# Performance work log

Measured on AMD Instinct MI355X. Metric: run time of the kernel, lower is better.

The kernel has to match this reference:

```python
import jax, jax.numpy as jnp
import numpy as np

N_NODES = 50000
N_EDGES = 1250000
IN_CH = 64
HID = 64
N_CLASSES = 10
N_GRAPHS = 128


def _xavier(key, shape):
    fan_out, fan_in = shape
    limit = np.sqrt(6.0 / (fan_in + fan_out))
    return jax.random.uniform(key, shape, jnp.float32, -limit, limit)


def setup_inputs() -> dict:
    key = jax.random.key(0)
    ks = jax.random.split(key, 12)
    x = jax.random.normal(ks[0], (N_NODES, IN_CH), jnp.float32)
    edge_index = jax.random.randint(ks[1], (2, N_EDGES), 0, N_NODES, jnp.int64)
    batch = jnp.sort(jax.random.randint(ks[2], (N_NODES,), 0, N_GRAPHS, jnp.int64))
    return {
        "x": x,
        "edge_index": edge_index,
        "batch": batch,
        # GraphConv i: lin_rel (weight+bias) applied to aggregated neighbors,
        # lin_root (no bias) applied to self features. Weights are [out, in].
        "W1_rel": _xavier(ks[3], (HID, IN_CH)), "b1": jnp.zeros((HID,), jnp.float32),
        "W1_root": _xavier(ks[4], (HID, IN_CH)),
        "W2_rel": _xavier(ks[5], (HID, HID)), "b2": jnp.zeros((HID,), jnp.float32),
        "W2_root": _xavier(ks[6], (HID, HID)),
        "W3_rel": _xavier(ks[7], (HID, HID)), "b3": jnp.zeros((HID,), jnp.float32),
        "W3_root": _xavier(ks[8], (HID, HID)),
        "W_lin": _xavier(ks[9], (N_CLASSES, HID)), "b_lin": jnp.zeros((N_CLASSES,), jnp.float32),
    }


def _graph_conv(x, src, dst, W_rel, b, W_root):
    # sum-aggregate neighbor features: gather at src, scatter-add at dst
    agg = jax.ops.segment_sum(x[src], dst, num_segments=N_NODES)  # [N, F]
    return agg @ W_rel.T + b + x @ W_root.T


def reference(x, edge_index, batch, W1_rel, b1, W1_root, W2_rel, b2, W2_root,
              W3_rel, b3, W3_root, W_lin, b_lin):
    src, dst = edge_index[0], edge_index[1]
    h = jax.nn.relu(_graph_conv(x, src, dst, W1_rel, b1, W1_root))
    h = jax.nn.relu(_graph_conv(h, src, dst, W2_rel, b2, W2_root))
    h = _graph_conv(h, src, dst, W3_rel, b3, W3_root)
    # global mean pool over graphs
    sums = jax.ops.segment_sum(h, batch, num_segments=N_GRAPHS)        # [G, HID]
    counts = jax.ops.segment_sum(jnp.ones((h.shape[0],), h.dtype), batch,
                                 num_segments=N_GRAPHS)
    pooled = sums / jnp.maximum(counts, 1.0)[:, None]
    out = pooled @ W_lin.T + b_lin  # dropout inactive in eval mode
    return (pooled, out)
```

## Files before the change

### kernel.cpp

```cpp
#include <hip/hip_runtime.h>

#define N_NODES   50000
#define HID       64
#define N_GRAPHS  128
#define N_CLASSES 10
#define NP        196
#define EPA       8192
#define PCAP      8192

typedef __attribute__((ext_vector_type(8))) short short8;
typedef __attribute__((ext_vector_type(4))) float f32x4;

__device__ __forceinline__ unsigned bf16rne(float f) {
    unsigned u = __float_as_uint(f);
    return (u + 0x7fffu + ((u >> 16) & 1u)) >> 16;
}
__device__ __forceinline__ unsigned pack_bf16x2(float lo, float hi) {
    return bf16rne(lo) | (bf16rne(hi) << 16);
}



__global__ void cvt_kernel(const float* __restrict__ x, unsigned short* __restrict__ xb,
                           int* __restrict__ gcursor) {
    if (blockIdx.x == 0 && threadIdx.x < NP) gcursor[threadIdx.x] = 0;
    int i = blockIdx.x * blockDim.x + threadIdx.x;
    if (i < N_NODES * 16) {
        float4 v = ((const float4*)x)[i];
        uint2 o;
        o.x = pack_bf16x2(v.x, v.y);
        o.y = pack_bf16x2(v.z, v.w);
        ((uint2*)xb)[i] = o;
    }
}


__global__ __launch_bounds__(256) void bucket_kernel(
    const int* __restrict__ src, const int* __restrict__ dst,
    int* __restrict__ gcursor, unsigned* __restrict__ packed, int E) {
    __shared__ int hist[NP], scp[NP], base[NP], cnt2[NP];
    __shared__ int sc[256];
    __shared__ unsigned stag[EPA];
    const int t = threadIdx.x;
    const int e0 = blockIdx.x * EPA;
    const int e1 = min(e0 + EPA, E);
    for (int i = t; i < NP; i += 256) { hist[i] = 0; cnt2[i] = 0; }
    __syncthreads();
    for (int e = e0 + t; e < e1; e += 256)
        atomicAdd(&hist[dst[e] >> 8], 1);
    __syncthreads();
    sc[t] = (t < NP) ? hist[t] : 0;
    __syncthreads();
    for (int off = 1; off < 256; off <<= 1) {
        int add = (t >= off) ? sc[t - off] : 0;
        __syncthreads();
        sc[t] += add;
        __syncthreads();
    }
    if (t < NP) {
        scp[t] = sc[t] - hist[t];
        if (hist[t] > 0) base[t] = atomicAdd(&gcursor[t], hist[t]);
    }
    __syncthreads();
    for (int e = e0 + t; e < e1; e += 256) {
        int d = dst[e], s = src[e];
        int p = d >> 8;
        int idx = scp[p] + atomicAdd(&cnt2[p], 1);
        stag[idx] = (unsigned)s | ((unsigned)(d & 255) << 16) | ((unsigned)p << 24);
    }
    __syncthreads();
    const int n = e1 - e0;
    for (int i = t; i < n; i += 256) {
        unsigned v = stag[i];
        int p = v >> 24;
        packed[(size_t)p * PCAP + base[p] + (i - scp[p])] = v & 0x00FFFFFFu;
    }
}

__global__ __launch_bounds__(256) void build_kernel(
    const unsigned* __restrict__ packed, const int* __restrict__ gcursor,
    int* __restrict__ offsets, unsigned short* __restrict__ csr,
    int* __restrict__ sums_zero) {
    __shared__ int hist[256], lofs[256], cnt[256], sc[256], gv[256];
    __shared__ unsigned short lcsr[PCAP];
    const int p = blockIdx.x, t = threadIdx.x;

    if (p == 0) {
        for (int i = t; i < N_GRAPHS * 64 + N_GRAPHS; i += 256) sums_zero[i] = 0;
    }

    int v = (t < NP) ? gcursor[t] : 0;
    sc[t] = v; gv[t] = v;
    __syncthreads();
    for (int off = 1; off < 256; off <<= 1) {
        int add = (t >= off) ? sc[t - off] : 0;
        __syncthreads();
        sc[t] += add;
        __syncthreads();
    }
    const int pb = sc[p] - gv[p];
    const int ne = gv[p];
    if (p == NP - 1 && t == 0) offsets[N_NODES] = sc[NP - 1];
    __syncthreads();

    const unsigned* mypk = packed + (size_t)p * PCAP;
    hist[t] = 0; cnt[t] = 0;
    __syncthreads();
    for (int i = t; i < ne; i += 256)
        atomicAdd(&hist[(mypk[i] >> 16) & 255], 1);
    __syncthreads();
    sc[t] = hist[t];
    __syncthreads();
    for (int off = 1; off < 256; off <<= 1) {
        int add = (t >= off) ? sc[t - off] : 0;
        __syncthreads();
        sc[t] += add;
        __syncthreads();
    }
    lofs[t] = sc[t] - hist[t];
    int node = p * 256 + t;
    if (node < N_NODES) offsets[node] = pb + lofs[t];
    __syncthreads();
    for (int i = t; i < ne; i += 256) {
        unsigned vv = mypk[i];
        int dl = (vv >> 16) & 255;
        int slot = lofs[dl] + atomicAdd(&cnt[dl], 1);
        lcsr[slot] = (unsigned short)(vv & 0xFFFFu);
    }
    __syncthreads();
    for (int i = t; i < ne; i += 256) csr[pb + i] = lcsr[i];
}


__global__ __launch_bounds__(256) void gather_kernel(
    const unsigned short* __restrict__ hin,
    const int* __restrict__ offsets, const unsigned short* __restrict__ csr_src,
    unsigned short* __restrict__ agg) {
    const int w = threadIdx.x >> 6, lane = threadIdx.x & 63;
    const int half = lane >> 5, hl = lane & 31;
    const int n = blockIdx.x * 4 + w;
    const int beg = offsets[n], end = offsets[n + 1];

    float accx = 0.f, accy = 0.f;
    for (int base = beg; base < end; base += 64) {
        int cnt = min(64, end - base);
        int sidx = (base + lane < end) ? (int)csr_src[base + lane] : 0;
        for (int kb = 0; kb < cnt; kb += 32) {
            unsigned u[16];
#pragma unroll
            for (int p = 0; p < 16; ++p) {
                int e = kb + 2 * p + half;
                int r = __shfl(sidx, e);
                u[p] = (e < cnt) ? *((const unsigned*)(hin + (size_t)r * 64) + hl) : 0u;
            }
#pragma unroll
            for (int p = 0; p < 16; ++p) {
                accx += __uint_as_float(u[p] << 16);
                accy += __uint_as_float(u[p] & 0xffff0000u);
            }
        }
    }
    float ox = accx + __shfl(accx, lane ^ 32);
    float oy = accy + __shfl(accy, lane ^ 32);
    if (half == 0)
        *((unsigned*)(agg + (size_t)n * 64) + hl) = pack_bf16x2(ox, oy);
}


template <int RELU>
__global__ __launch_bounds__(256) void linear_kernel(
    const unsigned short* __restrict__ agg,
    const unsigned short* __restrict__ hin,
    const float* __restrict__ Wrel, const float* __restrict__ bias,
    const float* __restrict__ Wroot, unsigned short* __restrict__ hout) {
    __shared__ unsigned short outT[4][16][72];

    const int tid = threadIdx.x;
    const int w = tid >> 6, lane = tid & 63;
    const int q = lane >> 4, c = lane & 15;
    const int g0 = (blockIdx.x * 4 + w) * 16;
    if (g0 >= N_NODES) return;

    short8 brel[4][2], broot[4][2];
    float biasv[4];
#pragma unroll
    for (int t = 0; t < 4; ++t) {
        int o = t * 16 + c;
        biasv[t] = bias[o];
#pragma unroll
        for (int s = 0; s < 2; ++s) {
            const float4* pr = (const float4*)(Wrel  + o * 64 + s * 32 + q * 8);
            const float4* po = (const float4*)(Wroot + o * 64 + s * 32 + q * 8);
            float4 r0 = pr[0], r1 = pr[1], z0 = po[0], z1 = po[1];
            short8 rr, zz;
            rr[0] = (short)bf16rne(r0.x); rr[1] = (short)bf16rne(r0.y);
            rr[2] = (short)bf16rne(r0.z); rr[3] = (short)bf16rne(r0.w);
            rr[4] = (short)bf16rne(r1.x); rr[5] = (short)bf16rne(r1.y);
            rr[6] = (short)bf16rne(r1.z); rr[7] = (short)bf16rne(r1.w);
            zz[0] = (short)bf16rne(z0.x); zz[1] = (short)bf16rne(z0.y);
            zz[2] = (short)bf16rne(z0.z); zz[3] = (short)bf16rne(z0.w);
            zz[4] = (short)bf16rne(z1.x); zz[5] = (short)bf16rne(z1.y);
            zz[6] = (short)bf16rne(z1.z); zz[7] = (short)bf16rne(z1.w);
            brel[t][s] = rr; broot[t][s] = zz;
        }
    }

    const int na = min(g0 + c, N_NODES - 1);
    short8 a_agg[2], a_x[2];
#pragma unroll
    for (int s = 0; s < 2; ++s) {
        a_agg[s] = *(const short8*)(agg + (size_t)na * 64 + s * 32 + q * 8);
        a_x[s]   = *(const short8*)(hin + (size_t)na * 64 + s * 32 + q * 8);
    }

    f32x4 acc4[4];
#pragma unroll
    for (int t = 0; t < 4; ++t) {
        f32x4 a0 = {biasv[t], biasv[t], biasv[t], biasv[t]};
        a0 = __builtin_amdgcn_mfma_f32_16x16x32_bf16(a_agg[0], brel[t][0], a0, 0, 0, 0);
        a0 = __builtin_amdgcn_mfma_f32_16x16x32_bf16(a_agg[1], brel[t][1], a0, 0, 0, 0);
        a0 = __builtin_amdgcn_mfma_f32_16x16x32_bf16(a_x[0],  broot[t][0], a0, 0, 0, 0);
        a0 = __builtin_amdgcn_mfma_f32_16x16x32_bf16(a_x[1],  broot[t][1], a0, 0, 0, 0);
        acc4[t] = a0;
    }

#pragma unroll
    for (int t = 0; t < 4; ++t)
#pragma unroll
        for (int r = 0; r < 4; ++r) {
            float v = acc4[t][r];
            if (RELU) v = fmaxf(v, 0.f);
            outT[w][q * 4 + r][t * 16 + c] = (unsigned short)bf16rne(v);
        }

#pragma unroll
    for (int it = 0; it < 2; ++it) {
        int row = it * 8 + (lane >> 3);
        int ch = (lane & 7) * 8;
        int n = g0 + row;
        if (n < N_NODES) {
            short8 v = *(const short8*)&outT[w][row][ch];
            *(short8*)(hout + (size_t)n * 64 + ch) = v;
        }
    }
}


__global__ __launch_bounds__(256) void pool_kernel(
    const unsigned short* __restrict__ h, const int* __restrict__ batch,
    float* __restrict__ sums, int* __restrict__ cnt) {
    int tid = threadIdx.x;
    int w = tid >> 6, lane = tid & 63;
    int n0 = blockIdx.x * 128 + w * 32;
    if (n0 >= N_NODES) return;
    int nend = min(n0 + 32, N_NODES);
    int cur = batch[n0];
    float acc = 0.f;
    int run = 0;
    for (int n = n0; n < nend; ++n) {
        int g = batch[n];
        if (g != cur) {
            atomicAdd(&sums[cur * 64 + lane], acc);
            if (lane == 0) atomicAdd(&cnt[cur], run);
            acc = 0.f; run = 0; cur = g;
        }
        unsigned u = h[(size_t)n * 64 + lane];
        acc += __uint_as_float(u << 16);
        run++;
    }
    atomicAdd(&sums[cur * 64 + lane], acc);
    if (lane == 0) atomicAdd(&cnt[cur], run);
}

__global__ void final_kernel(const float* __restrict__ sums, const int* __restrict__ cnt,
                             const float* __restrict__ Wlin, const float* __restrict__ blin,
                             float* __restrict__ out) {
    __shared__ float pl[64];
    int g = blockIdx.x, lane = threadIdx.x;
    float cdiv = fmaxf((float)cnt[g], 1.0f);
    float p = sums[g * 64 + lane] / cdiv;
    out[g * 64 + lane] = p;
    pl[lane] = p;
    __syncthreads();
    if (lane < N_CLASSES) {
        float o = blin[lane];
#pragma unroll
        for (int k = 0; k < 64; ++k) o += pl[k] * Wlin[lane * 64 + k];
        out[N_GRAPHS * 64 + g * N_CLASSES + lane] = o;
    }
}


extern "C" void kernel_launch(void* const* d_in, const int* in_sizes, int n_in,
                              void* d_out, int out_size, void* d_ws, size_t ws_size,
                              hipStream_t stream) {
    const float* x     = (const float*)d_in[0];
    const int*   ei    = (const int*)d_in[1];
    const int*   batch = (const int*)d_in[2];
    const float* W1r = (const float*)d_in[3];
    const float* b1  = (const float*)d_in[4];
    const float* W1o = (const float*)d_in[5];
    const float* W2r = (const float*)d_in[6];
    const float* b2  = (const float*)d_in[7];
    const float* W2o = (const float*)d_in[8];
    const float* W3r = (const float*)d_in[9];
    const float* b3  = (const float*)d_in[10];
    const float* W3o = (const float*)d_in[11];
    const float* Wl  = (const float*)d_in[12];
    const float* bl  = (const float*)d_in[13];
    float* out = (float*)d_out;

    const int E = in_sizes[1] / 2;
    const int* src = ei;
    const int* dst = ei + E;

    char* p = (char*)d_ws;
    unsigned short* xb  = (unsigned short*)p; p += (size_t)N_NODES * 64 * 2;
    unsigned short* h1  = (unsigned short*)p; p += (size_t)N_NODES * 64 * 2;
    unsigned short* h2  = (unsigned short*)p; p += (size_t)N_NODES * 64 * 2;
    unsigned short* agg = (unsigned short*)p; p += (size_t)N_NODES * 64 * 2;
    unsigned short* h3  = h1;
    unsigned* packed    = (unsigned*)p; p += (size_t)NP * PCAP * 4;
    unsigned short* csr = (unsigned short*)p; p += (size_t)E * 2;
    int* offsets   = (int*)p;   p += (size_t)(N_NODES + 1) * 4;
    int* gcursor   = (int*)p;   p += NP * 4;
    float* sums    = (float*)p; p += (size_t)N_GRAPHS * 64 * 4;
    int* cnt       = (int*)p;   p += N_GRAPHS * 4;

    const int NCHUNK = (E + EPA - 1) / EPA;
    cvt_kernel<<<(N_NODES * 16 + 255) / 256, 256, 0, stream>>>(x, xb, gcursor);
    bucket_kernel<<<NCHUNK, 256, 0, stream>>>(src, dst, gcursor, packed, E);
    build_kernel<<<NP, 256, 0, stream>>>(packed, gcursor, offsets, csr, (int*)sums);

    const int GB = N_NODES / 4;
    const int LB = (N_NODES + 63) / 64;
    gather_kernel<<<GB, 256, 0, stream>>>(xb, offsets, csr, agg);
    linear_kernel<1><<<LB, 256, 0, stream>>>(agg, xb, W1r, b1, W1o, h1);
    gather_kernel<<<GB, 256, 0, stream>>>(h1, offsets, csr, agg);
    linear_kernel<1><<<LB, 256, 0, stream>>>(agg, h1, W2r, b2, W2o, h2);
    gather_kernel<<<GB, 256, 0, stream>>>(h2, offsets, csr, agg);
    linear_kernel<0><<<LB, 256, 0, stream>>>(agg, h2, W3r, b3, W3o, h3);

    pool_kernel<<<(N_NODES + 127) / 128, 256, 0, stream>>>(h3, batch, sums, cnt);
    final_kernel<<<N_GRAPHS, 64, 0, stream>>>(sums, cnt, Wl, bl, out);
}
```

Baseline: 266.9 us.

## Fuse neighbor gather with linear MFMA per layer and merge pooling kernels

Each GraphConv layer becomes one kernel. A 1024-thread block gathers 16 nodes' neighbor sums into shared memory, then four waves run the bf16 MFMA linear step on those rows, so the aggregate no longer makes a global-memory round trip. Pooling now binary-searches each graph's node range in the sorted batch array and reduces it in one block per graph, which removes the atomics, the zeroing pass and the separate final kernel. The cost is that the linear stage has only 4 of 16 waves active, each block reconverts the weights to bf16, and the large blocks may lower occupancy.

```diff
diff --git a/kernel.cpp b/kernel.cpp
--- a/kernel.cpp
+++ b/kernel.cpp
@@ -18,7 +18,6 @@
 __device__ __forceinline__ unsigned pack_bf16x2(float lo, float hi) {
     return bf16rne(lo) | (bf16rne(hi) << 16);
 }
-
 
 
 __global__ void cvt_kernel(const float* __restrict__ x, unsigned short* __restrict__ xb,
@@ -79,15 +78,10 @@
 
 __global__ __launch_bounds__(256) void build_kernel(
     const unsigned* __restrict__ packed, const int* __restrict__ gcursor,
-    int* __restrict__ offsets, unsigned short* __restrict__ csr,
-    int* __restrict__ sums_zero) {
+    int* __restrict__ offsets, unsigned short* __restrict__ csr) {
     __shared__ int hist[256], lofs[256], cnt[256], sc[256], gv[256];
     __shared__ unsigned short lcsr[PCAP];
     const int p = blockIdx.x, t = threadIdx.x;
-
-    if (p == 0) {
-        for (int i = t; i < N_GRAPHS * 64 + N_GRAPHS; i += 256) sums_zero[i] = 0;
-    }
 
     int v = (t < NP) ? gcursor[t] : 0;
     sc[t] = v; gv[t] = v;
@@ -132,15 +126,22 @@
 }
 
 
-__global__ __launch_bounds__(256) void gather_kernel(
+template <int RELU>
+__global__ __launch_bounds__(1024) void layer_kernel(
     const unsigned short* __restrict__ hin,
     const int* __restrict__ offsets, const unsigned short* __restrict__ csr_src,
-    unsigned short* __restrict__ agg) {
-    const int w = threadIdx.x >> 6, lane = threadIdx.x & 63;
+    const float* __restrict__ Wrel, const float* __restrict__ bias,
+    const float* __restrict__ Wroot, unsigned short* __restrict__ hout) {
+    __shared__ unsigned short aggT[16][72];
+    __shared__ unsigned short outT[16][72];
+
+    const int tid = threadIdx.x;
+    const int w = tid >> 6, lane = tid & 63;
     const int half = lane >> 5, hl = lane & 31;
-    const int n = blockIdx.x * 4 + w;
+    const int g0 = blockIdx.x * 16;
+    const int n = g0 + w;
+
     const int beg = offsets[n], end = offsets[n + 1];
-
     float accx = 0.f, accy = 0.f;
     for (int base = beg; base < end; base += 64) {
         int cnt = min(64, end - base);
@@ -163,30 +164,14 @@
     float ox = accx + __shfl(accx, lane ^ 32);
     float oy = accy + __shfl(accy, lane ^ 32);
     if (half == 0)
-        *((unsigned*)(agg + (size_t)n * 64) + hl) = pack_bf16x2(ox, oy);
-}
-
-
-template <int RELU>
-__global__ __launch_bounds__(256) void linear_kernel(
-    const unsigned short* __restrict__ agg,
-    const unsigned short* __restrict__ hin,
-    const float* __restrict__ Wrel, const float* __restrict__ bias,
-    const float* __restrict__ Wroot, unsigned short* __restrict__ hout) {
-    __shared__ unsigned short outT[4][16][72];
-
-    const int tid = threadIdx.x;
-    const int w = tid >> 6, lane = tid & 63;
-    const int q = lane >> 4, c = lane & 15;
-    const int g0 = (blockIdx.x * 4 + w) * 16;
-    if (g0 >= N_NODES) return;
-
-    short8 brel[4][2], broot[4][2];
-    float biasv[4];
-#pragma unroll
-    for (int t = 0; t < 4; ++t) {
-        int o = t * 16 + c;
-        biasv[t] = bias[o];
+        *((unsigned*)&aggT[w][0] + hl) = pack_bf16x2(ox, oy);
+    __syncthreads();
+
+    if (w < 4) {
+        const int q = lane >> 4, c = lane & 15;
+        const int o = w * 16 + c;
+        const float biasv = bias[o];
+        short8 brel_[2], broot_[2];
 #pragma unroll
         for (int s = 0; s < 2; ++s) {
             const float4* pr = (const float4*)(Wrel  + o * 64 + s * 32 + q * 8);
@@ -201,92 +186,72 @@
             zz[2] = (short)bf16rne(z0.z); zz[3] = (short)bf16rne(z0.w);
             zz[4] = (short)bf16rne(z1.x); zz[5] = (short)bf16rne(z1.y);
             zz[6] = (short)bf16rne(z1.z); zz[7] = (short)bf16rne(z1.w);
-            brel[t][s] = rr; broot[t][s] = zz;
+            brel_[s] = rr; broot_[s] = zz;
         }
-    }
-
-    const int na = min(g0 + c, N_NODES - 1);
-    short8 a_agg[2], a_x[2];
-#pragma unroll
-    for (int s = 0; s < 2; ++s) {
-        a_agg[s] = *(const short8*)(agg + (size_t)na * 64 + s * 32 + q * 8);
-        a_x[s]   = *(const short8*)(hin + (size_t)na * 64 + s * 32 + q * 8);
-    }
-
-    f32x4 acc4[4];
-#pragma unroll
-    for (int t = 0; t < 4; ++t) {
-        f32x4 a0 = {biasv[t], biasv[t], biasv[t], biasv[t]};
-        a0 = __builtin_amdgcn_mfma_f32_16x16x32_bf16(a_agg[0], brel[t][0], a0, 0, 0, 0);
-        a0 = __builtin_amdgcn_mfma_f32_16x16x32_bf16(a_agg[1], brel[t][1], a0, 0, 0, 0);
-        a0 = __builtin_amdgcn_mfma_f32_16x16x32_bf16(a_x[0],  broot[t][0], a0, 0, 0, 0);
-        a0 = __builtin_amdgcn_mfma_f32_16x16x32_bf16(a_x[1],  broot[t][1], a0, 0, 0, 0);
-        acc4[t] = a0;
-    }
-
-#pragma unroll
-    for (int t = 0; t < 4; ++t)
+        short8 a_agg[2], a_x[2];
+#pragma unroll
+        for (int s = 0; s < 2; ++s) {
+            a_agg[s] = *(const short8*)&aggT[c][s * 32 + q * 8];
+            a_x[s]   = *(const short8*)(hin + (size_t)(g0 + c) * 64 + s * 32 + q * 8);
+        }
+        f32x4 a0 = {biasv, biasv, biasv, biasv};
+        a0 = __builtin_amdgcn_mfma_f32_16x16x32_bf16(a_agg[0], brel_[0], a0, 0, 0, 0);
+        a0 = __builtin_amdgcn_mfma_f32_16x16x32_bf16(a_agg[1], brel_[1], a0, 0, 0, 0);
+        a0 = __builtin_amdgcn_mfma_f32_16x16x32_bf16(a_x[0],  broot_[0], a0, 0, 0, 0);
+        a0 = __builtin_amdgcn_mfma_f32_16x16x32_bf16(a_x[1],  broot_[1], a0, 0, 0, 0);
 #pragma unroll
         for (int r = 0; r < 4; ++r) {
-            float v = acc4[t][r];
+            float v = a0[r];
             if (RELU) v = fmaxf(v, 0.f);
-            outT[w][q * 4 + r][t * 16 + c] = (unsigned short)bf16rne(v);
+            outT[q * 4 + r][w * 16 + c] = (unsigned short)bf16rne(v);
         }
-
-#pragma unroll
-    for (int it = 0; it < 2; ++it) {
-        int row = it * 8 + (lane >> 3);
-        int ch = (lane & 7) * 8;
-        int n = g0 + row;
-        if (n < N_NODES) {
-            short8 v = *(const short8*)&outT[w][row][ch];
-            *(short8*)(hout + (size_t)n * 64 + ch) = v;
-        }
-    }
-}
-
-
-__global__ __launch_bounds__(256) void pool_kernel(
+    }
+    __syncthreads();
+
+    if (tid < 128) {
+        int row = tid >> 3;
+        int ch = (tid & 7) * 8;
+        short8 v = *(const short8*)&outT[row][ch];
+        *(short8*)(hout + (size_t)(g0 + row) * 64 + ch) = v;
+    }
+}
+
+
+__global__ __launch_bounds__(256) void poolfinal_kernel(
     const unsigned short* __restrict__ h, const int* __restrict__ batch,
-    float* __restrict__ sums, int* __restrict__ cnt) {
-    int tid = threadIdx.x;
-    int w = tid >> 6, lane = tid & 63;
-    int n0 = blockIdx.x * 128 + w * 32;
-    if (n0 >= N_NODES) return;
-    int nend = min(n0 + 32, N_NODES);
-    int cur = batch[n0];
+    const float* __restrict__ Wlin, const float* __restrict__ blin,
+    float* __restrict__ out) {
+    __shared__ float part[4][64];
+    const int g = blockIdx.x;
+    const int tid = threadIdx.x, w = tid >> 6, lane = tid & 63;
+
+    int a = 0, b = N_NODES;
+    while (a < b) { int m = (a + b) >> 1; if (batch[m] < g) a = m + 1; else b = m; }
+    const int lo = a;
+    b = N_NODES;
+    while (a < b) { int m = (a + b) >> 1; if (batch[m] < g + 1) a = m + 1; else b = m; }
+    const int hi = a;
+
     float acc = 0.f;
-    int run = 0;
-    for (int n = n0; n < nend; ++n) {
-        int g = batch[n];
-        if (g != cur) {
-            atomicAdd(&sums[cur * 64 + lane], acc);
-            if (lane == 0) atomicAdd(&cnt[cur], run);
-            acc = 0.f; run = 0; cur = g;
-        }
+    for (int n = lo + w; n < hi; n += 4) {
         unsigned u = h[(size_t)n * 64 + lane];
         acc += __uint_as_float(u << 16);
-        run++;
-    }
-    atomicAdd(&sums[cur * 64 + lane], acc);
-    if (lane == 0) atomicAdd(&cnt[cur], run);
-}
-
-__global__ void final_kernel(const float* __restrict__ sums, const int* __restrict__ cnt,
-                             const float* __restrict__ Wlin, const float* __restrict__ blin,
-                             float* __restrict__ out) {
-    __shared__ float pl[64];
-    int g = blockIdx.x, lane = threadIdx.x;
-    float cdiv = fmaxf((float)cnt[g], 1.0f);
-    float p = sums[g * 64 + lane] / cdiv;
-    out[g * 64 + lane] = p;
-    pl[lane] = p;
-    __syncthreads();
-    if (lane < N_CLASSES) {
-        float o = blin[lane];
-#pragma unroll
-        for (int k = 0; k < 64; ++k) o += pl[k] * Wlin[lane * 64 + k];
-        out[N_GRAPHS * 64 + g * N_CLASSES + lane] = o;
+    }
+    part[w][lane] = acc;
+    __syncthreads();
+    if (w == 0) {
+        float s = part[0][lane] + part[1][lane] + part[2][lane] + part[3][lane];
+        float cdiv = fmaxf((float)(hi - lo), 1.0f);
+        float pv = s / cdiv;
+        out[g * 64 + lane] = pv;
+        part[0][lane] = pv;
+    }
+    __syncthreads();
+    if (tid < N_CLASSES) {
+        float o = blin[tid];
+#pragma unroll
+        for (int k = 0; k < 64; ++k) o += part[0][k] * Wlin[tid * 64 + k];
+        out[N_GRAPHS * 64 + g * N_CLASSES + tid] = o;
     }
 }
 
@@ -318,29 +283,21 @@
     unsigned short* xb  = (unsigned short*)p; p += (size_t)N_NODES * 64 * 2;
     unsigned short* h1  = (unsigned short*)p; p += (size_t)N_NODES * 64 * 2;
     unsigned short* h2  = (unsigned short*)p; p += (size_t)N_NODES * 64 * 2;
-    unsigned short* agg = (unsigned short*)p; p += (size_t)N_NODES * 64 * 2;
     unsigned short* h3  = h1;
     unsigned* packed    = (unsigned*)p; p += (size_t)NP * PCAP * 4;
     unsigned short* csr = (unsigned short*)p; p += (size_t)E * 2;
     int* offsets   = (int*)p;   p += (size_t)(N_NODES + 1) * 4;
     int* gcursor   = (int*)p;   p += NP * 4;
-    float* sums    = (float*)p; p += (size_t)N_GRAPHS * 64 * 4;
-    int* cnt       = (int*)p;   p += N_GRAPHS * 4;
 
     const int NCHUNK = (E + EPA - 1) / EPA;
     cvt_kernel<<<(N_NODES * 16 + 255) / 256, 256, 0, stream>>>(x, xb, gcursor);
     bucket_kernel<<<NCHUNK, 256, 0, stream>>>(src, dst, gcursor, packed, E);
-    build_kernel<<<NP, 256, 0, stream>>>(packed, gcursor, offsets, csr, (int*)sums);
-
-    const int GB = N_NODES / 4;
-    const int LB = (N_NODES + 63) / 64;
-    gather_kernel<<<GB, 256, 0, stream>>>(xb, offsets, csr, agg);
-    linear_kernel<1><<<LB, 256, 0, stream>>>(agg, xb, W1r, b1, W1o, h1);
-    gather_kernel<<<GB, 256, 0, stream>>>(h1, offsets, csr, agg);
-    linear_kernel<1><<<LB, 256, 0, stream>>>(agg, h1, W2r, b2, W2o, h2);
-    gather_kernel<<<GB, 256, 0, stream>>>(h2, offsets, csr, agg);
-    linear_kernel<0><<<LB, 256, 0, stream>>>(agg, h2, W3r, b3, W3o, h3);
-
-    pool_kernel<<<(N_NODES + 127) / 128, 256, 0, stream>>>(h3, batch, sums, cnt);
-    final_kernel<<<N_GRAPHS, 64, 0, stream>>>(sums, cnt, Wl, bl, out);
-}
+    build_kernel<<<NP, 256, 0, stream>>>(packed, gcursor, offsets, csr);
+
+    const int LB = N_NODES / 16;
+    layer_kernel<1><<<LB, 1024, 0, stream>>>(xb, offsets, csr, W1r, b1, W1o, h1);
+    layer_kernel<1><<<LB, 1024, 0, stream>>>(h1, offsets, csr, W2r, b2, W2o, h2);
+    layer_kernel<0><<<LB, 1024, 0, stream>>>(h2, offsets, csr, W3r, b3, W3o, h3);
+
+    poolfinal_kernel<<<N_GRAPHS, 256, 0, stream>>>(h3, batch, Wl, bl, out);
+}
```

Result: slower. 275.4 us (+3.2%).

## Fuse pooling and final linear into one per-graph kernel; add nontemporal hints

Applied to the files above, without the earlier changes.

Replaces the atomic-based pool kernel and the separate final kernel with one kernel launched per graph. Each block binary-searches the sorted batch array for its node range, sums features across four waves, then computes the mean and the classifier output. This removes the zeroing of sums in build_kernel, the atomics and one launch. It also adds nontemporal load/store hints on the CSR indices and the agg buffer. With only 128 blocks the pooling step may underuse the GPU and is sensitive to uneven graph sizes.

```diff
diff --git a/kernel.cpp b/kernel.cpp
--- a/kernel.cpp
+++ b/kernel.cpp
@@ -18,7 +18,6 @@
 __device__ __forceinline__ unsigned pack_bf16x2(float lo, float hi) {
     return bf16rne(lo) | (bf16rne(hi) << 16);
 }
-
 
 
 __global__ void cvt_kernel(const float* __restrict__ x, unsigned short* __restrict__ xb,
@@ -79,15 +78,10 @@
 
 __global__ __launch_bounds__(256) void build_kernel(
     const unsigned* __restrict__ packed, const int* __restrict__ gcursor,
-    int* __restrict__ offsets, unsigned short* __restrict__ csr,
-    int* __restrict__ sums_zero) {
+    int* __restrict__ offsets, unsigned short* __restrict__ csr) {
     __shared__ int hist[256], lofs[256], cnt[256], sc[256], gv[256];
     __shared__ unsigned short lcsr[PCAP];
     const int p = blockIdx.x, t = threadIdx.x;
-
-    if (p == 0) {
-        for (int i = t; i < N_GRAPHS * 64 + N_GRAPHS; i += 256) sums_zero[i] = 0;
-    }
 
     int v = (t < NP) ? gcursor[t] : 0;
     sc[t] = v; gv[t] = v;
@@ -144,7 +138,7 @@
     float accx = 0.f, accy = 0.f;
     for (int base = beg; base < end; base += 64) {
         int cnt = min(64, end - base);
-        int sidx = (base + lane < end) ? (int)csr_src[base + lane] : 0;
+        int sidx = (base + lane < end) ? (int)__builtin_nontemporal_load(&csr_src[base + lane]) : 0;
         for (int kb = 0; kb < cnt; kb += 32) {
             unsigned u[16];
 #pragma unroll
@@ -163,7 +157,8 @@
     float ox = accx + __shfl(accx, lane ^ 32);
     float oy = accy + __shfl(accy, lane ^ 32);
     if (half == 0)
-        *((unsigned*)(agg + (size_t)n * 64) + hl) = pack_bf16x2(ox, oy);
+        __builtin_nontemporal_store(pack_bf16x2(ox, oy),
+                                    (unsigned*)(agg + (size_t)n * 64) + hl);
 }
 
 
@@ -209,7 +204,7 @@
     short8 a_agg[2], a_x[2];
 #pragma unroll
     for (int s = 0; s < 2; ++s) {
-        a_agg[s] = *(const short8*)(agg + (size_t)na * 64 + s * 32 + q * 8);
+        a_agg[s] = __builtin_nontemporal_load((const short8*)(agg + (size_t)na * 64 + s * 32 + q * 8));
         a_x[s]   = *(const short8*)(hin + (size_t)na * 64 + s * 32 + q * 8);
     }
 
@@ -246,47 +241,41 @@
 }
 
 
-__global__ __launch_bounds__(256) void pool_kernel(
+__global__ __launch_bounds__(256) void poolfinal_kernel(
     const unsigned short* __restrict__ h, const int* __restrict__ batch,
-    float* __restrict__ sums, int* __restrict__ cnt) {
-    int tid = threadIdx.x;
-    int w = tid >> 6, lane = tid & 63;
-    int n0 = blockIdx.x * 128 + w * 32;
-    if (n0 >= N_NODES) return;
-    int nend = min(n0 + 32, N_NODES);
-    int cur = batch[n0];
+    const float* __restrict__ Wlin, const float* __restrict__ blin,
+    float* __restrict__ out) {
+    __shared__ float part[4][64];
+    const int g = blockIdx.x;
+    const int tid = threadIdx.x, w = tid >> 6, lane = tid & 63;
+
+    int a = 0, b = N_NODES;
+    while (a < b) { int m = (a + b) >> 1; if (batch[m] < g) a = m + 1; else b = m; }
+    const int lo = a;
+    b = N_NODES;
+    while (a < b) { int m = (a + b) >> 1; if (batch[m] < g + 1) a = m + 1; else b = m; }
+    const int hi = a;
+
     float acc = 0.f;
-    int run = 0;
-    for (int n = n0; n < nend; ++n) {
-        int g = batch[n];
-        if (g != cur) {
-            atomicAdd(&sums[cur * 64 + lane], acc);
-            if (lane == 0) atomicAdd(&cnt[cur], run);
-            acc = 0.f; run = 0; cur = g;
-        }
-        unsigned u = h[(size_t)n * 64 + lane];
-        acc += __uint_as_float(u << 16);
-        run++;
-    }
-    atomicAdd(&sums[cur * 64 + lane], acc);
-    if (lane == 0) atomicAdd(&cnt[cur], run);
-}
-
-__global__ void final_kernel(const float* __restrict__ sums, const int* __restrict__ cnt,
-                             const float* __restrict__ Wlin, const float* __restrict__ blin,
-                             float* __restrict__ out) {
-    __shared__ float pl[64];
-    int g = blockIdx.x, lane = threadIdx.x;
-    float cdiv = fmaxf((float)cnt[g], 1.0f);
-    float p = sums[g * 64 + lane] / cdiv;
-    out[g * 64 + lane] = p;
-    pl[lane] = p;
-    __syncthreads();
-    if (lane < N_CLASSES) {
-        float o = blin[lane];
-#pragma unroll
-        for (int k = 0; k < 64; ++k) o += pl[k] * Wlin[lane * 64 + k];
-        out[N_GRAPHS * 64 + g * N_CLASSES + lane] = o;
+    for (int n = lo + w; n < hi; n += 4) {
+        unsigned u = __builtin_nontemporal_load(h + (size_t)n * 64 + lane);
+        acc += __uint_as_float((unsigned)u << 16);
+    }
+    part[w][lane] = acc;
+    __syncthreads();
+    if (w == 0) {
+        float s = part[0][lane] + part[1][lane] + part[2][lane] + part[3][lane];
+        float cdiv = fmaxf((float)(hi - lo), 1.0f);
+        float pv = s / cdiv;
+        out[g * 64 + lane] = pv;
+        part[0][lane] = pv;
+    }
+    __syncthreads();
+    if (tid < N_CLASSES) {
+        float o = blin[tid];
+#pragma unroll
+        for (int k = 0; k < 64; ++k) o += part[0][k] * Wlin[tid * 64 + k];
+        out[N_GRAPHS * 64 + g * N_CLASSES + tid] = o;
     }
 }
 
@@ -324,13 +313,11 @@
     unsigned short* csr = (unsigned short*)p; p += (size_t)E * 2;
     int* offsets   = (int*)p;   p += (size_t)(N_NODES + 1) * 4;
     int* gcursor   = (int*)p;   p += NP * 4;
-    float* sums    = (float*)p; p += (size_t)N_GRAPHS * 64 * 4;
-    int* cnt       = (int*)p;   p += N_GRAPHS * 4;
 
     const int NCHUNK = (E + EPA - 1) / EPA;
     cvt_kernel<<<(N_NODES * 16 + 255) / 256, 256, 0, stream>>>(x, xb, gcursor);
     bucket_kernel<<<NCHUNK, 256, 0, stream>>>(src, dst, gcursor, packed, E);
-    build_kernel<<<NP, 256, 0, stream>>>(packed, gcursor, offsets, csr, (int*)sums);
+    build_kernel<<<NP, 256, 0, stream>>>(packed, gcursor, offsets, csr);
 
     const int GB = N_NODES / 4;
     const int LB = (N_NODES + 63) / 64;
@@ -341,6 +328,5 @@
     gather_kernel<<<GB, 256, 0, stream>>>(h2, offsets, csr, agg);
     linear_kernel<0><<<LB, 256, 0, stream>>>(agg, h2, W3r, b3, W3o, h3);
 
-    pool_kernel<<<(N_NODES + 127) / 128, 256, 0, stream>>>(h3, batch, sums, cnt);
-    final_kernel<<<N_GRAPHS, 64, 0, stream>>>(sums, cnt, Wl, bl, out);
-}
+    poolfinal_kernel<<<N_GRAPHS, 256, 0, stream>>>(h3, batch, Wl, bl, out);
+}
```

Result: slower. 288.9 us (+8.3%).
